# Performance work log

Hardware: AMD Instinct MI355X
Metric: run time of the kernel (lower is better)

Reference implementation:

```python
import jax, jax.numpy as jnp
import numpy as np

# Model dims (match init_kwargs)
B, S, DIN, DIM = 1, 4096, 1024, 1024
NH, NKV = 16, 4
HD = DIM // NH          # head_dim = 64
GS = NH // NKV          # group_size = 4 (query heads per KV group)


def setup_inputs() -> dict:
    key = jax.random.key(0)
    ks = jax.random.split(key, 5)
    def w(k, shape, fan_in):
        return jax.random.normal(k, shape, jnp.float32) * (fan_in ** -0.5)
    return {
        "x": jax.random.normal(ks[0], (B, S, DIN), jnp.float32),
        "wq": w(ks[1], (DIM, DIN), DIN),            # nn.Linear(din, dim)
        "wk": w(ks[2], (NKV * HD, DIN), DIN),       # nn.Linear(din, nkv*hd)
        "wv": w(ks[3], (NKV * HD, DIN), DIN),
        "wo": w(ks[4], (DIM, DIM), DIM),            # output proj
    }


def reference(x, wq, wk, wv, wo):
    b, s, _ = x.shape
    # Projections (Linear: x @ W^T, bias=False)
    # Query head h = g*GS + m uses KV group g -> reshape heads as (g, m),
    # which is exactly repeat_interleave(group_size) on K/V without copying.
    q = (x @ wq.T).reshape(b, s, NKV, GS, HD)   # [b, s, g, m, d]
    k = (x @ wk.T).reshape(b, s, NKV, HD)       # [b, s, g, d]
    v = (x @ wv.T).reshape(b, s, NKV, HD)
    scale = jnp.asarray(HD ** 0.5, x.dtype)
    att = jnp.einsum('bsgmd,btgd->bgmst', q, k) / scale  # [b, g, m, s, s]
    causal = jnp.triu(jnp.ones((s, s), bool), 1)
    att = jnp.where(causal, -jnp.inf, att)
    att = jax.nn.softmax(att, axis=-1)          # dropout p=0.0 -> identity
    ctx = jnp.einsum('bgmst,btgd->bsgmd', att, v).reshape(b, s, DIM)
    return ctx @ wo.T
```

## Files before the change

kernel.cpp:

```cpp
#include <hip/hip_runtime.h>

typedef __bf16 bf16_t;
typedef __bf16 bf16x8 __attribute__((ext_vector_type(8)));
typedef float  f32x4  __attribute__((ext_vector_type(4)));

#define MFMA16(a, b, c) __builtin_amdgcn_mfma_f32_16x16x32_bf16((a), (b), (c), 0, 0, 0)

__device__ __forceinline__ void gload_lds16(const void* g, void* l) {
  __builtin_amdgcn_global_load_lds((__attribute__((address_space(1))) void*)(g),
                                   (__attribute__((address_space(3))) void*)(l),
                                   16, 0, 0);
}

__global__ __launch_bounds__(256) void cvt_all(const float* __restrict__ x,
                                               const float* __restrict__ wq,
                                               const float* __restrict__ wk,
                                               const float* __restrict__ wv,
                                               const float* __restrict__ wo,
                                               bf16_t* __restrict__ xb,
                                               bf16_t* __restrict__ wqkv,
                                               bf16_t* __restrict__ wob) {
  int i = (blockIdx.x * 256 + threadIdx.x) * 8;
  const float* src;
  bf16_t* dst;
  int off;
  if (i < 4194304)      { src = x;  dst = xb;             off = i; }
  else if (i < 5242880) { src = wq; dst = wqkv;           off = i - 4194304; }
  else if (i < 5505024) { src = wk; dst = wqkv + 1048576; off = i - 5242880; }
  else if (i < 5767168) { src = wv; dst = wqkv + 1310720; off = i - 5505024; }
  else                  { src = wo; dst = wob;            off = i - 5767168; }
  const float4* pp = reinterpret_cast<const float4*>(src + off);
  float4 a = pp[0], b = pp[1];
  bf16x8 v;
  v[0] = (bf16_t)a.x; v[1] = (bf16_t)a.y; v[2] = (bf16_t)a.z; v[3] = (bf16_t)a.w;
  v[4] = (bf16_t)b.x; v[5] = (bf16_t)b.y; v[6] = (bf16_t)b.z; v[7] = (bf16_t)b.w;
  *reinterpret_cast<bf16x8*>(dst + off) = v;
}

template <typename T>
__global__ __launch_bounds__(256) void gemm_bt(const bf16_t* __restrict__ A,
                                               const bf16_t* __restrict__ B,
                                               T* __restrict__ C,
                                               int M, int N, int K,
                                               bf16_t* __restrict__ kp,
                                               bf16_t* __restrict__ vt) {
  constexpr int BK = 64;
  int tid  = threadIdx.x;
  int lane = tid & 63, w = tid >> 6;
  int wr = w >> 1, wc = w & 1;
  int l15 = lane & 15, lhi = lane >> 4;
  int row0 = blockIdx.y * 128, col0 = blockIdx.x * 128;

  __shared__ alignas(16) char smem[128 * BK * 2 * 2];
  char* sA = smem;
  char* sB = smem + 128 * BK * 2;

  f32x4 acc[4][4] = {};

  for (int k0 = 0; k0 < K; k0 += BK) {
#pragma unroll
    for (int i = 0; i < 4; ++i) {
      int c = i * 256 + tid;
      int r = c >> 3, kc = c & 7;
      int kk = k0 + ((kc ^ (r & 7)) << 3);
      gload_lds16(A + (size_t)(row0 + r) * K + kk, sA + c * 16);
      gload_lds16(B + (size_t)(col0 + r) * K + kk, sB + c * 16);
    }
    __syncthreads();
#pragma unroll
    for (int s = 0; s < 2; ++s) {
      bf16x8 af[4], bfr[4];
#pragma unroll
      for (int mi = 0; mi < 4; ++mi) {
        int r = wr * 64 + mi * 16 + l15;
        af[mi] = *reinterpret_cast<const bf16x8*>(
            sA + r * 128 + (((s * 4 + lhi) ^ (r & 7)) << 4));
      }
#pragma unroll
      for (int nj = 0; nj < 4; ++nj) {
        int r = wc * 64 + nj * 16 + l15;
        bfr[nj] = *reinterpret_cast<const bf16x8*>(
            sB + r * 128 + (((s * 4 + lhi) ^ (r & 7)) << 4));
      }
#pragma unroll
      for (int mi = 0; mi < 4; ++mi)
#pragma unroll
        for (int nj = 0; nj < 4; ++nj)
          acc[mi][nj] = MFMA16(af[mi], bfr[nj], acc[mi][nj]);
    }
    __syncthreads();
  }

  const float KSCALE = 0.18033688f;
#pragma unroll
  for (int mi = 0; mi < 4; ++mi)
#pragma unroll
    for (int nj = 0; nj < 4; ++nj) {
      int colb = col0 + wc * 64 + nj * 16 + l15;
      int rowb = row0 + wr * 64 + mi * 16 + lhi * 4;
      if (kp != nullptr && colb >= 1024) {
        if (colb < 1280) {
          int gg = (colb - 1024) >> 6, d = (colb - 1024) & 63;
          bf16_t* kdst = kp + ((size_t)gg * 4096 + rowb) * 64 + d;
#pragma unroll
          for (int r2 = 0; r2 < 4; ++r2)
            kdst[r2 * 64] = (bf16_t)(acc[mi][nj][r2] * KSCALE);
        } else {
          union { bf16_t hh[4]; uint64_t u; } a;
#pragma unroll
          for (int r2 = 0; r2 < 4; ++r2) a.hh[r2] = (bf16_t)acc[mi][nj][r2];
          *reinterpret_cast<uint64_t*>(vt + (size_t)(colb - 1280) * 4096 + rowb) = a.u;
        }
      } else {
#pragma unroll
        for (int r2 = 0; r2 < 4; ++r2)
          C[(size_t)(rowb + r2) * N + colb] = (T)acc[mi][nj][r2];
      }
    }
}

__global__ __launch_bounds__(256, 2) void attn_kernel(const bf16_t* __restrict__ qkv,
                                                      const bf16_t* __restrict__ kp,
                                                      const bf16_t* __restrict__ vt,
                                                      bf16_t* __restrict__ ctx) {
  int tid = threadIdx.x, lane = tid & 63, w = tid >> 6;
  int l15 = lane & 15, lhi = lane >> 4;
  int bid = blockIdx.x;
  int pos = bid & 15, p = bid >> 4;
  int g = (pos & 7) >> 1;
  int h = g * 4 + (((pos >> 3) << 1) | (pos & 1));

  __shared__ alignas(16) char kv[2][16384];
  __shared__ alignas(16) char pb_all[4][2304];
  char* pbuf = pb_all[w];

  const bf16_t* kbase = kp + (size_t)g * 4096 * 64;
  const bf16_t* vbase = vt + (size_t)g * 64 * 4096;

  auto STAGE = [&](int j0, int b) {
#pragma unroll
    for (int i = 0; i < 2; ++i) {
      int c = i * 256 + tid;
      int r = c >> 3, kc = c & 7;
      int d8 = kc ^ (r & 7);
      gload_lds16(kbase + (size_t)(j0 + r) * 64 + d8 * 8, &kv[b][c * 16]);
    }
#pragma unroll
    for (int i = 0; i < 2; ++i) {
      int c = i * 256 + tid;
      int r = c >> 3, kc = c & 7;
      int d8 = kc ^ (r & 7);
      gload_lds16(vbase + (size_t)r * 4096 + j0 + d8 * 8, &kv[b][8192 + c * 16]);
    }
  };

  auto runTile = [&](int tile) {
    int r0 = tile * 64;
    int wr0 = r0 + w * 16;
    int nsteps = tile + 1;

    bf16x8 qf[2];
#pragma unroll
    for (int ks = 0; ks < 2; ++ks)
      qf[ks] = *reinterpret_cast<const bf16x8*>(
          qkv + (size_t)(wr0 + l15) * 1536 + h * 64 + ks * 32 + lhi * 8);

    f32x4 O[4] = {};
    float lsum = 0.f;

    STAGE(0, 0);
    __syncthreads();

    for (int step = 0; step < nsteps; ++step) {
      int b = step & 1;
      if (step + 1 < nsteps) STAGE((step + 1) * 64, b ^ 1);
      int j0 = step * 64;
      const char* kt  = kv[b];
      const char* vtl = kv[b] + 8192;
      bool diag = (j0 + 64 > r0);
#pragma unroll
      for (int nj = 0; nj < 4; ++nj) {
        int kr = nj * 16 + l15;
        const char* krow = kt + kr * 128;
        bf16x8 k0 = *reinterpret_cast<const bf16x8*>(krow + ((lhi ^ (kr & 7)) << 4));
        bf16x8 k1 = *reinterpret_cast<const bf16x8*>(krow + (((4 + lhi) ^ (kr & 7)) << 4));
        f32x4 t = {0.f, 0.f, 0.f, 0.f};
        t = MFMA16(k0, qf[0], t);
        t = MFMA16(k1, qf[1], t);
        if (diag) {
          int qr = wr0 + l15;
#pragma unroll
          for (int r = 0; r < 4; ++r) {
            int key = j0 + nj * 16 + lhi * 4 + r;
            if (key > qr) t[r] = -1e30f;
          }
        }
        int cofs = (nj * 2 + (lhi >> 1)) * 16 + ((lhi & 1) << 3);
        union { bf16_t hh[4]; uint64_t u; } a;
        float ls = 0.f;
#pragma unroll
        for (int r = 0; r < 4; ++r) {
          float pv = exp2f(t[r]);
          ls += pv;
          a.hh[r] = (bf16_t)pv;
        }
        lsum += ls;
        *reinterpret_cast<uint64_t*>(pbuf + l15 * 144 + cofs) = a.u;
      }
      bf16x8 ap[2];
#pragma unroll
      for (int ks = 0; ks < 2; ++ks)
        ap[ks] = *reinterpret_cast<const bf16x8*>(
            pbuf + l15 * 144 + ((ks * 4 + lhi) << 4));
#pragma unroll
      for (int h4 = 0; h4 < 4; ++h4) {
        int vr = h4 * 16 + l15;
        const char* vrow = vtl + vr * 128;
        bf16x8 v0 = *reinterpret_cast<const bf16x8*>(vrow + ((lhi ^ (vr & 7)) << 4));
        bf16x8 v1 = *reinterpret_cast<const bf16x8*>(vrow + (((4 + lhi) ^ (vr & 7)) << 4));
        O[h4] = MFMA16(ap[0], v0, O[h4]);
        O[h4] = MFMA16(ap[1], v1, O[h4]);
      }
      __syncthreads();
    }

    lsum += __shfl_xor(lsum, 16);
    lsum += __shfl_xor(lsum, 32);
    float il[4];
#pragma unroll
    for (int r = 0; r < 4; ++r)
      il[r] = 1.0f / __shfl(lsum, lhi * 4 + r);
#pragma unroll
    for (int h4 = 0; h4 < 4; ++h4)
#pragma unroll
      for (int r = 0; r < 4; ++r) {
        int row = wr0 + lhi * 4 + r;
        ctx[(size_t)row * 1024 + h * 64 + h4 * 16 + l15] =
            (bf16_t)(O[h4][r] * il[r]);
      }
  };

  runTile(63 - p);
  __syncthreads();
  runTile(p);
}

extern "C" void kernel_launch(void* const* d_in, const int* in_sizes, int n_in,
                              void* d_out, int out_size, void* d_ws, size_t ws_size,
                              hipStream_t stream) {
  const float* x  = (const float*)d_in[0];
  const float* wq = (const float*)d_in[1];
  const float* wk = (const float*)d_in[2];
  const float* wv = (const float*)d_in[3];
  const float* wo = (const float*)d_in[4];
  float* out = (float*)d_out;

  char* ws = (char*)d_ws;
  size_t off = 0;
  auto alloc = [&](size_t b) {
    char* p = ws + off;
    off += (b + 255) & ~(size_t)255;
    return p;
  };
  bf16_t* wob  = (bf16_t*)alloc((size_t)1024 * 1024 * 2);
  bf16_t* qkv  = (bf16_t*)alloc((size_t)4096 * 1536 * 2);
  bf16_t* vtb  = (bf16_t*)alloc((size_t)256 * 4096 * 2);
  bf16_t* kpb  = (bf16_t*)alloc((size_t)4 * 4096 * 64 * 2);
  bf16_t* ctx  = (bf16_t*)alloc((size_t)4096 * 1024 * 2);
  bf16_t* xb   = (bf16_t*)alloc((size_t)4096 * 1024 * 2);
  bf16_t* wqkv = (bf16_t*)alloc((size_t)1536 * 1024 * 2);

  cvt_all<<<3328, 256, 0, stream>>>(x, wq, wk, wv, wo, xb, wqkv, wob);
  gemm_bt<bf16_t><<<dim3(12, 32), 256, 0, stream>>>(xb, wqkv, qkv, 4096, 1536, 1024,
                                                    kpb, vtb);
  attn_kernel<<<512, 256, 0, stream>>>(qkv, kpb, vtb, ctx);
  gemm_bt<float><<<dim3(8, 32), 256, 0, stream>>>(ctx, wob, out, 4096, 1024, 1024,
                                                  nullptr, nullptr);
}
```

Baseline: 133.9 us.

## Split long causal attention tiles across two blocks and combine partials

Doubles the attention grid. Long query tiles (index above 32) have their key range split at step 33: one block handles the first 33 key tiles and another handles the remainder plus a short paired tile. Unnormalized fp32 partial outputs and row sums go to scratch, and a new combine kernel sums and normalizes them into ctx. The intent is to raise parallelism and balance load on the GPU, at the cost of an extra launch and extra global traffic for the partials. The P buffer also switches from padding to an XOR swizzle, which shrinks LDS per wave.

Measured after the change: 127.5 us (median of 2 runs). 1.05x faster.

```diff
diff --git a/kernel.cpp b/kernel.cpp
--- a/kernel.cpp
+++ b/kernel.cpp
@@ -122,16 +122,20 @@
 __global__ __launch_bounds__(256, 2) void attn_kernel(const bf16_t* __restrict__ qkv,
                                                       const bf16_t* __restrict__ kp,
                                                       const bf16_t* __restrict__ vt,
-                                                      bf16_t* __restrict__ ctx) {
+                                                      bf16_t* __restrict__ ctx,
+                                                      float* __restrict__ Opart,
+                                                      float* __restrict__ lpart) {
   int tid = threadIdx.x, lane = tid & 63, w = tid >> 6;
   int l15 = lane & 15, lhi = lane >> 4;
+  int e = l15 & 7;
   int bid = blockIdx.x;
-  int pos = bid & 15, p = bid >> 4;
+  int pos = bid & 15, qq = bid >> 4;
+  int p = qq >> 1, half = qq & 1;
   int g = (pos & 7) >> 1;
   int h = g * 4 + (((pos >> 3) << 1) | (pos & 1));
 
   __shared__ alignas(16) char kv[2][16384];
-  __shared__ alignas(16) char pb_all[4][2304];
+  __shared__ alignas(16) char pb_all[4][2048];
   char* pbuf = pb_all[w];
 
   const bf16_t* kbase = kp + (size_t)g * 4096 * 64;
@@ -154,10 +158,10 @@
     }
   };
 
-  auto runTile = [&](int tile) {
+  auto runPhase = [&](int tile, int sbeg, int send, bool fin,
+                      float* Oslot, float* lslot) {
     int r0 = tile * 64;
     int wr0 = r0 + w * 16;
-    int nsteps = tile + 1;
 
     bf16x8 qf[2];
 #pragma unroll
@@ -168,12 +172,12 @@
     f32x4 O[4] = {};
     float lsum = 0.f;
 
-    STAGE(0, 0);
+    STAGE(sbeg * 64, 0);
     __syncthreads();
 
-    for (int step = 0; step < nsteps; ++step) {
-      int b = step & 1;
-      if (step + 1 < nsteps) STAGE((step + 1) * 64, b ^ 1);
+    for (int step = sbeg; step < send; ++step) {
+      int b = (step - sbeg) & 1;
+      if (step + 1 < send) STAGE((step + 1) * 64, b ^ 1);
       int j0 = step * 64;
       const char* kt  = kv[b];
       const char* vtl = kv[b] + 8192;
@@ -195,7 +199,7 @@
             if (key > qr) t[r] = -1e30f;
           }
         }
-        int cofs = (nj * 2 + (lhi >> 1)) * 16 + ((lhi & 1) << 3);
+        int sw = (nj * 2 + (lhi >> 1)) ^ e;
         union { bf16_t hh[4]; uint64_t u; } a;
         float ls = 0.f;
 #pragma unroll
@@ -205,13 +209,13 @@
           a.hh[r] = (bf16_t)pv;
         }
         lsum += ls;
-        *reinterpret_cast<uint64_t*>(pbuf + l15 * 144 + cofs) = a.u;
+        *reinterpret_cast<uint64_t*>(pbuf + l15 * 128 + sw * 16 + ((lhi & 1) << 3)) = a.u;
       }
       bf16x8 ap[2];
 #pragma unroll
       for (int ks = 0; ks < 2; ++ks)
         ap[ks] = *reinterpret_cast<const bf16x8*>(
-            pbuf + l15 * 144 + ((ks * 4 + lhi) << 4));
+            pbuf + l15 * 128 + (((ks * 4 + lhi) ^ e) << 4));
 #pragma unroll
       for (int h4 = 0; h4 < 4; ++h4) {
         int vr = h4 * 16 + l15;
@@ -226,23 +230,71 @@
 
     lsum += __shfl_xor(lsum, 16);
     lsum += __shfl_xor(lsum, 32);
-    float il[4];
-#pragma unroll
-    for (int r = 0; r < 4; ++r)
-      il[r] = 1.0f / __shfl(lsum, lhi * 4 + r);
-#pragma unroll
-    for (int h4 = 0; h4 < 4; ++h4)
-#pragma unroll
-      for (int r = 0; r < 4; ++r) {
-        int row = wr0 + lhi * 4 + r;
-        ctx[(size_t)row * 1024 + h * 64 + h4 * 16 + l15] =
-            (bf16_t)(O[h4][r] * il[r]);
-      }
+    if (fin) {
+      float il[4];
+#pragma unroll
+      for (int r = 0; r < 4; ++r)
+        il[r] = 1.0f / __shfl(lsum, lhi * 4 + r);
+#pragma unroll
+      for (int h4 = 0; h4 < 4; ++h4)
+#pragma unroll
+        for (int r = 0; r < 4; ++r) {
+          int row = wr0 + lhi * 4 + r;
+          ctx[(size_t)row * 1024 + h * 64 + h4 * 16 + l15] =
+              (bf16_t)(O[h4][r] * il[r]);
+        }
+    } else {
+      if (lhi == 0) lslot[w * 16 + l15] = lsum;
+#pragma unroll
+      for (int h4 = 0; h4 < 4; ++h4)
+#pragma unroll
+        for (int r = 0; r < 4; ++r)
+          Oslot[(size_t)(w * 16 + lhi * 4 + r) * 64 + h4 * 16 + l15] = O[h4][r];
+    }
   };
 
-  runTile(63 - p);
-  __syncthreads();
-  runTile(p);
+  if (half == 0) {
+    bool fin = (p == 31);
+    if (fin) {
+      runPhase(63 - p, 0, 33, true, nullptr, nullptr);
+    } else {
+      int u = (30 - p) * 16 + h;
+      runPhase(63 - p, 0, 33, false,
+               Opart + ((size_t)u * 2 + 0) * 4096, lpart + ((size_t)u * 2 + 0) * 64);
+    }
+  } else {
+    if (p < 31) {
+      int u = (30 - p) * 16 + h;
+      runPhase(63 - p, 33, 64 - p, false,
+               Opart + ((size_t)u * 2 + 1) * 4096, lpart + ((size_t)u * 2 + 1) * 64);
+    }
+    runPhase(p, 0, p + 1, true, nullptr, nullptr);
+  }
+}
+
+__global__ __launch_bounds__(256) void norm_combine(const float* __restrict__ Opart,
+                                                    const float* __restrict__ lpart,
+                                                    bf16_t* __restrict__ ctx) {
+  int u = blockIdx.x;
+  int T = 33 + (u >> 4), h = u & 15;
+  int t = threadIdx.x;
+  int row = t >> 2, q = t & 3;
+  const float* O0 = Opart + (size_t)u * 2 * 4096;
+  const float* O1 = O0 + 4096;
+  const float* l0 = lpart + (size_t)u * 2 * 64;
+  const float* l1 = l0 + 64;
+  float il = 1.0f / (l0[row] + l1[row]);
+#pragma unroll
+  for (int i = 0; i < 4; ++i) {
+    int idx = row * 64 + q * 16 + i * 4;
+    f32x4 a = *reinterpret_cast<const f32x4*>(O0 + idx);
+    f32x4 b = *reinterpret_cast<const f32x4*>(O1 + idx);
+    union { bf16_t hh[4]; uint64_t uu; } o;
+#pragma unroll
+    for (int r = 0; r < 4; ++r) o.hh[r] = (bf16_t)((a[r] + b[r]) * il);
+    *reinterpret_cast<uint64_t*>(
+        ctx + (size_t)(T * 64 + row) * 1024 + h * 64 + q * 16 + i * 4) = o.uu;
+  }
 }
 
 extern "C" void kernel_launch(void* const* d_in, const int* in_sizes, int n_in,
@@ -267,13 +319,17 @@
   bf16_t* vtb  = (bf16_t*)alloc((size_t)256 * 4096 * 2);
   bf16_t* kpb  = (bf16_t*)alloc((size_t)4 * 4096 * 64 * 2);
   bf16_t* ctx  = (bf16_t*)alloc((size_t)4096 * 1024 * 2);
+  size_t scratch_base = off;
   bf16_t* xb   = (bf16_t*)alloc((size_t)4096 * 1024 * 2);
   bf16_t* wqkv = (bf16_t*)alloc((size_t)1536 * 1024 * 2);
+  float* Opart = (float*)(ws + scratch_base);
+  float* lpart = Opart + (size_t)496 * 2 * 4096;
 
   cvt_all<<<3328, 256, 0, stream>>>(x, wq, wk, wv, wo, xb, wqkv, wob);
   gemm_bt<bf16_t><<<dim3(12, 32), 256, 0, stream>>>(xb, wqkv, qkv, 4096, 1536, 1024,
                                                     kpb, vtb);
-  attn_kernel<<<512, 256, 0, stream>>>(qkv, kpb, vtb, ctx);
+  attn_kernel<<<1024, 256, 0, stream>>>(qkv, kpb, vtb, ctx, Opart, lpart);
+  norm_combine<<<496, 256, 0, stream>>>(Opart, lpart, ctx);
   gemm_bt<float><<<dim3(8, 32), 256, 0, stream>>>(ctx, wob, out, 4096, 1024, 1024,
                                                   nullptr, nullptr);
 }
```

## Share K/V tile staging between paired query tiles and compute row sums via MFMA

Applied to the files above, without the earlier changes.

Each block previously processed its two causal query tiles (63-p and p) one after the other, staging K/V from key 0 twice. The attention loop now runs once over 64-p key tiles and applies each staged K/V tile to both query tiles, with the short tile active only for the first p+1 steps. This roughly halves K/V global-to-LDS traffic and the number of barriers. Row sums of P are now computed with an MFMA against a ones vector instead of scalar adds and shuffles, and the P buffer uses an XOR swizzle instead of padding. The cost is more registers for two accumulator sets, which may reduce occupancy under launch_bounds(256,2).

After: 132.8 us. No clear change (-0.8%).

```diff
diff --git a/kernel.cpp b/kernel.cpp
--- a/kernel.cpp
+++ b/kernel.cpp
@@ -125,14 +125,18 @@
                                                       bf16_t* __restrict__ ctx) {
   int tid = threadIdx.x, lane = tid & 63, w = tid >> 6;
   int l15 = lane & 15, lhi = lane >> 4;
+  int e = l15 & 7;
   int bid = blockIdx.x;
   int pos = bid & 15, p = bid >> 4;
   int g = (pos & 7) >> 1;
   int h = g * 4 + (((pos >> 3) << 1) | (pos & 1));
+  int A = 63 - p;
+  int nstage = 64 - p;
 
   __shared__ alignas(16) char kv[2][16384];
-  __shared__ alignas(16) char pb_all[4][2304];
-  char* pbuf = pb_all[w];
+  __shared__ alignas(16) char pb_all[4][4096];
+  char* pbufA = pb_all[w];
+  char* pbufB = pb_all[w] + 2048;
 
   const bf16_t* kbase = kp + (size_t)g * 4096 * 64;
   const bf16_t* vbase = vt + (size_t)g * 64 * 4096;
@@ -154,29 +158,37 @@
     }
   };
 
-  auto runTile = [&](int tile) {
-    int r0 = tile * 64;
-    int wr0 = r0 + w * 16;
-    int nsteps = tile + 1;
-
-    bf16x8 qf[2];
-#pragma unroll
-    for (int ks = 0; ks < 2; ++ks)
-      qf[ks] = *reinterpret_cast<const bf16x8*>(
-          qkv + (size_t)(wr0 + l15) * 1536 + h * 64 + ks * 32 + lhi * 8);
-
-    f32x4 O[4] = {};
-    float lsum = 0.f;
-
-    STAGE(0, 0);
-    __syncthreads();
-
-    for (int step = 0; step < nsteps; ++step) {
-      int b = step & 1;
-      if (step + 1 < nsteps) STAGE((step + 1) * 64, b ^ 1);
-      int j0 = step * 64;
-      const char* kt  = kv[b];
-      const char* vtl = kv[b] + 8192;
+  int r0A = A * 64, wr0A = r0A + w * 16;
+  int r0B = p * 64, wr0B = r0B + w * 16;
+
+  bf16x8 qfA[2], qfB[2];
+#pragma unroll
+  for (int ks = 0; ks < 2; ++ks) {
+    qfA[ks] = *reinterpret_cast<const bf16x8*>(
+        qkv + (size_t)(wr0A + l15) * 1536 + h * 64 + ks * 32 + lhi * 8);
+    qfB[ks] = *reinterpret_cast<const bf16x8*>(
+        qkv + (size_t)(wr0B + l15) * 1536 + h * 64 + ks * 32 + lhi * 8);
+  }
+
+  bf16x8 ones;
+#pragma unroll
+  for (int i = 0; i < 8; ++i) ones[i] = (bf16_t)1.0f;
+
+  f32x4 OA[4] = {}, OB[4] = {};
+  f32x4 lA = {0.f, 0.f, 0.f, 0.f}, lB = {0.f, 0.f, 0.f, 0.f};
+
+  STAGE(0, 0);
+  __syncthreads();
+
+  for (int step = 0; step < nstage; ++step) {
+    int b = step & 1;
+    if (step + 1 < nstage) STAGE((step + 1) * 64, b ^ 1);
+    int j0 = step * 64;
+    const char* kt  = kv[b];
+    const char* vtl = kv[b] + 8192;
+
+    auto TILE = [&](int r0, int wr0, const bf16x8 (&qf)[2], char* pbuf,
+                    f32x4 (&O)[4], f32x4& lacc) {
       bool diag = (j0 + 64 > r0);
 #pragma unroll
       for (int nj = 0; nj < 4; ++nj) {
@@ -195,23 +207,19 @@
             if (key > qr) t[r] = -1e30f;
           }
         }
-        int cofs = (nj * 2 + (lhi >> 1)) * 16 + ((lhi & 1) << 3);
+        int sw = (nj * 2 + (lhi >> 1)) ^ e;
         union { bf16_t hh[4]; uint64_t u; } a;
-        float ls = 0.f;
-#pragma unroll
-        for (int r = 0; r < 4; ++r) {
-          float pv = exp2f(t[r]);
-          ls += pv;
-          a.hh[r] = (bf16_t)pv;
-        }
-        lsum += ls;
-        *reinterpret_cast<uint64_t*>(pbuf + l15 * 144 + cofs) = a.u;
+#pragma unroll
+        for (int r = 0; r < 4; ++r) a.hh[r] = (bf16_t)exp2f(t[r]);
+        *reinterpret_cast<uint64_t*>(pbuf + l15 * 128 + sw * 16 + ((lhi & 1) << 3)) = a.u;
       }
       bf16x8 ap[2];
 #pragma unroll
       for (int ks = 0; ks < 2; ++ks)
         ap[ks] = *reinterpret_cast<const bf16x8*>(
-            pbuf + l15 * 144 + ((ks * 4 + lhi) << 4));
+            pbuf + l15 * 128 + (((ks * 4 + lhi) ^ e) << 4));
+      lacc = MFMA16(ap[0], ones, lacc);
+      lacc = MFMA16(ap[1], ones, lacc);
 #pragma unroll
       for (int h4 = 0; h4 < 4; ++h4) {
         int vr = h4 * 16 + l15;
@@ -221,28 +229,31 @@
         O[h4] = MFMA16(ap[0], v0, O[h4]);
         O[h4] = MFMA16(ap[1], v1, O[h4]);
       }
-      __syncthreads();
-    }
-
-    lsum += __shfl_xor(lsum, 16);
-    lsum += __shfl_xor(lsum, 32);
-    float il[4];
-#pragma unroll
-    for (int r = 0; r < 4; ++r)
-      il[r] = 1.0f / __shfl(lsum, lhi * 4 + r);
-#pragma unroll
-    for (int h4 = 0; h4 < 4; ++h4)
-#pragma unroll
-      for (int r = 0; r < 4; ++r) {
-        int row = wr0 + lhi * 4 + r;
-        ctx[(size_t)row * 1024 + h * 64 + h4 * 16 + l15] =
-            (bf16_t)(O[h4][r] * il[r]);
-      }
-  };
-
-  runTile(63 - p);
-  __syncthreads();
-  runTile(p);
+    };
+
+    TILE(r0A, wr0A, qfA, pbufA, OA, lA);
+    if (step <= p)
+      TILE(r0B, wr0B, qfB, pbufB, OB, lB);
+
+    __syncthreads();
+  }
+
+#pragma unroll
+  for (int h4 = 0; h4 < 4; ++h4)
+#pragma unroll
+    for (int r = 0; r < 4; ++r) {
+      int row = wr0A + lhi * 4 + r;
+      ctx[(size_t)row * 1024 + h * 64 + h4 * 16 + l15] =
+          (bf16_t)(OA[h4][r] / lA[r]);
+    }
+#pragma unroll
+  for (int h4 = 0; h4 < 4; ++h4)
+#pragma unroll
+    for (int r = 0; r < 4; ++r) {
+      int row = wr0B + lhi * 4 + r;
+      ctx[(size_t)row * 1024 + h * 64 + h4 * 16 + l15] =
+          (bf16_t)(OB[h4][r] / lB[r]);
+    }
 }
 
 extern "C" void kernel_launch(void* const* d_in, const int* in_sizes, int n_in,
```
